# Optimization experiments

Measured on AMD Instinct MI355X. Metric: run time of the kernel, lower is better.

The kernel has to match this reference:

```python
import jax, jax.numpy as jnp
import numpy as np

NUM_PRIMITIVES = 1024
DIM = 1024
TAU = 0.5  # temperature used by LivingCodebook.discretize default


def setup_inputs() -> dict:
    key = jax.random.key(0)
    k1, k2 = jax.random.split(key)
    logits = jax.random.normal(k1, (8, 4096, NUM_PRIMITIVES), dtype=jnp.float32)
    # learned codebook (nn.Parameter torch.randn(K, D) * 0.02)
    primitives = jax.random.normal(k2, (NUM_PRIMITIVES, DIM), dtype=jnp.float32) * 0.02
    return {"logits": logits, "primitives": primitives}


def _gumbel_softmax_hard(logits, key, tau):
    # F.gumbel_softmax(logits, tau, hard=True): straight-through one-hot
    g = jax.random.gumbel(key, logits.shape, dtype=logits.dtype)
    y_soft = jax.nn.softmax((logits + g) / tau, axis=-1)  # [b,s,k]
    idx = jnp.argmax(y_soft, axis=-1)                     # [b,s]
    y_hard = jax.nn.one_hot(idx, logits.shape[-1], dtype=logits.dtype)
    # hard forward value, soft gradient
    y = y_hard + y_soft - jax.lax.stop_gradient(y_soft)
    return y, idx


def reference(logits, primitives):
    """LivingCodebook.discretize: hard gumbel-softmax selection + codebook gather
    (expressed as one-hot GEMM for straight-through grads), plus the
    activation_count update vectorized as a scatter-add."""
    noise_key = jax.random.key(42)
    weights, indices = _gumbel_softmax_hard(logits, noise_key, TAU)
    # embeddings = weights @ primitives : [b,s,k] x [k,d] -> [b,s,d]
    embeddings = jnp.einsum("bsk,kd->bsd", weights, primitives)
    # activation_count[idx] += 1 for every selected index (vectorized)
    counts = jnp.zeros((primitives.shape[0],), dtype=jnp.int32).at[indices.reshape(-1)].add(1)
    return embeddings, indices, counts
```

## Files before the change

### kernel.cpp

```cpp
#include <hip/hip_runtime.h>
#include <stdint.h>

#define NROWS   32768
#define KDIM    1024
#define IDX_OFF 33554432
#define CNT_OFF 33587200

__device__ __forceinline__ uint32_t rotl32(uint32_t x, int r) {
    return (x << r) | (x >> (32 - r));
}

__device__ __forceinline__ uint32_t threefry_bits(uint32_t ctr) {
    const uint32_t ks0 = 0u;
    const uint32_t ks1 = 42u;
    const uint32_t ks2 = 0x1BD11BDAu ^ 0u ^ 42u;

    uint32_t x0 = 0u + ks0;
    uint32_t x1 = ctr + ks1;

    x0 += x1; x1 = rotl32(x1, 13); x1 ^= x0;
    x0 += x1; x1 = rotl32(x1, 15); x1 ^= x0;
    x0 += x1; x1 = rotl32(x1, 26); x1 ^= x0;
    x0 += x1; x1 = rotl32(x1,  6); x1 ^= x0;
    x0 += ks1; x1 += ks2 + 1u;
    x0 += x1; x1 = rotl32(x1, 17); x1 ^= x0;
    x0 += x1; x1 = rotl32(x1, 29); x1 ^= x0;
    x0 += x1; x1 = rotl32(x1, 16); x1 ^= x0;
    x0 += x1; x1 = rotl32(x1, 24); x1 ^= x0;
    x0 += ks2; x1 += ks0 + 2u;
    x0 += x1; x1 = rotl32(x1, 13); x1 ^= x0;
    x0 += x1; x1 = rotl32(x1, 15); x1 ^= x0;
    x0 += x1; x1 = rotl32(x1, 26); x1 ^= x0;
    x0 += x1; x1 = rotl32(x1,  6); x1 ^= x0;
    x0 += ks0; x1 += ks1 + 3u;
    x0 += x1; x1 = rotl32(x1, 17); x1 ^= x0;
    x0 += x1; x1 = rotl32(x1, 29); x1 ^= x0;
    x0 += x1; x1 = rotl32(x1, 16); x1 ^= x0;
    x0 += x1; x1 = rotl32(x1, 24); x1 ^= x0;
    x0 += ks1; x1 += ks2 + 4u;
    x0 += x1; x1 = rotl32(x1, 13); x1 ^= x0;
    x0 += x1; x1 = rotl32(x1, 15); x1 ^= x0;
    x0 += x1; x1 = rotl32(x1, 26); x1 ^= x0;
    x0 += x1; x1 = rotl32(x1,  6); x1 ^= x0;
    x0 += ks2; x1 += ks0 + 5u;

    return x0 ^ x1;
}

__device__ __forceinline__ float score_from_bits(uint32_t bits, float logit) {
    float v1 = __uint_as_float((bits >> 9) | 0x3f800000u);
    float f  = v1 - 1.0f;
    float u  = fmaxf(f, 1.17549435e-38f);
    float w  = u - 1.0f;
    float q;
    q = fmaf(w, -0.20609929f,  0.24044917f);
    q = fmaf(w, q, -0.28853901f);
    q = fmaf(w, q,  0.36067376f);
    q = fmaf(w, q, -0.48089835f);
    q = fmaf(w, q,  0.72134752f);
    q = fmaf(w, q, -1.44269504f);
    float tp = w * q;
    float th = -__builtin_amdgcn_logf(u);
    float t  = (u >= 0.875f) ? tp : th;
    float lg = __builtin_amdgcn_logf(t);
    return fmaf(logit, 1.44269504f, -lg);
}

__global__ __launch_bounds__(256) void gumbel_argmax_gather(
    const float* __restrict__ logits,
    const float* __restrict__ prim,
    float* __restrict__ out)
{
    const int row = blockIdx.x;
    const int tid = threadIdx.x;
    const uint32_t base = (uint32_t)row * (uint32_t)KDIM;
    const uint32_t k0   = 4u * (uint32_t)tid;

    const float4 l4 = *reinterpret_cast<const float4*>(logits + base + k0);
    const float lv[4] = {l4.x, l4.y, l4.z, l4.w};

    float bv = -INFINITY;
    int   bk = 0;
    #pragma unroll
    for (int m = 0; m < 4; ++m) {
        const float z = score_from_bits(threefry_bits(base + k0 + (uint32_t)m), lv[m]);
        if (z > bv) { bv = z; bk = (int)k0 + m; }
    }

    #pragma unroll
    for (int off = 32; off > 0; off >>= 1) {
        const float ov = __shfl_down(bv, off);
        const int   ok = __shfl_down(bk, off);
        if (ov > bv || (ov == bv && ok < bk)) { bv = ov; bk = ok; }
    }

    __shared__ float s_v[4];
    __shared__ int   s_k[4];
    __shared__ int   s_idx;
    const int wave = tid >> 6;
    if ((tid & 63) == 0) { s_v[wave] = bv; s_k[wave] = bk; }
    __syncthreads();

    if (tid == 0) {
        float v = s_v[0]; int kk = s_k[0];
        #pragma unroll
        for (int w = 1; w < 4; ++w) {
            if (s_v[w] > v || (s_v[w] == v && s_k[w] < kk)) { v = s_v[w]; kk = s_k[w]; }
        }
        s_idx = kk;
        out[IDX_OFF + row] = (float)kk;
        atomicAdd(out + CNT_OFF + kk, 1.0f);
    }
    __syncthreads();

    const int idx = s_idx;
    const float4* __restrict__ src = (const float4*)(prim + (size_t)idx * KDIM);
    float4* __restrict__ dst = (float4*)(out + (size_t)row * KDIM);
    dst[tid] = src[tid];
}

extern "C" void kernel_launch(void* const* d_in, const int* in_sizes, int n_in,
                              void* d_out, int out_size, void* d_ws, size_t ws_size,
                              hipStream_t stream) {
    const float* logits = (const float*)d_in[0];
    const float* prim   = (const float*)d_in[1];
    float* out = (float*)d_out;
    (void)d_ws; (void)ws_size; (void)in_sizes; (void)n_in; (void)out_size;

    hipMemsetAsync(out + CNT_OFF, 0, KDIM * sizeof(float), stream);
    gumbel_argmax_gather<<<NROWS, 256, 0, stream>>>(logits, prim, out);
}
```

Before: 242.6 us.

## Assign one wavefront per row and drop block-level argmax synchronisation

Each 64-lane wavefront now processes a whole row: it scans all 1024 logits in four coalesced float4 passes and reduces with xor shuffles, so the shared-memory staging and both __syncthreads are gone. The grid shrinks to a quarter as many blocks, and every lane copies four float4 chunks of the selected codebook row. The uniform-variate math is also simplified, using an integer mantissa compare and computing w from v1 directly, which drops the fmax clamp. The cost is more serial work per thread and more registers, and the branch threshold and clamp semantics shift slightly for zero mantissas.

```diff
diff --git a/kernel.cpp b/kernel.cpp
--- a/kernel.cpp
+++ b/kernel.cpp
@@ -48,10 +48,10 @@
 }
 
 __device__ __forceinline__ float score_from_bits(uint32_t bits, float logit) {
-    float v1 = __uint_as_float((bits >> 9) | 0x3f800000u);
-    float f  = v1 - 1.0f;
-    float u  = fmaxf(f, 1.17549435e-38f);
-    float w  = u - 1.0f;
+    const uint32_t m  = bits >> 9;
+    const float    v1 = __uint_as_float(m | 0x3f800000u);
+    const float    u  = v1 - 1.0f;
+    const float    w  = v1 - 2.0f;
     float q;
     q = fmaf(w, -0.20609929f,  0.24044917f);
     q = fmaf(w, q, -0.28853901f);
@@ -59,10 +59,10 @@
     q = fmaf(w, q, -0.48089835f);
     q = fmaf(w, q,  0.72134752f);
     q = fmaf(w, q, -1.44269504f);
-    float tp = w * q;
-    float th = -__builtin_amdgcn_logf(u);
-    float t  = (u >= 0.875f) ? tp : th;
-    float lg = __builtin_amdgcn_logf(t);
+    const float tp = w * q;
+    const float th = -__builtin_amdgcn_logf(u);
+    const float t  = (m >= 0x00700000u) ? tp : th;
+    const float lg = __builtin_amdgcn_logf(t);
     return fmaf(logit, 1.44269504f, -lg);
 }
 
@@ -71,52 +71,52 @@
     const float* __restrict__ prim,
     float* __restrict__ out)
 {
-    const int row = blockIdx.x;
-    const int tid = threadIdx.x;
+    const int tid  = threadIdx.x;
+    const int lane = tid & 63;
+    const int wv   = tid >> 6;
+    const int row  = (blockIdx.x << 2) + wv;
     const uint32_t base = (uint32_t)row * (uint32_t)KDIM;
-    const uint32_t k0   = 4u * (uint32_t)tid;
 
-    const float4 l4 = *reinterpret_cast<const float4*>(logits + base + k0);
-    const float lv[4] = {l4.x, l4.y, l4.z, l4.w};
+    float bv[4] = {-INFINITY, -INFINITY, -INFINITY, -INFINITY};
+    int   bk[4] = {0, 0, 0, 0};
 
-    float bv = -INFINITY;
-    int   bk = 0;
     #pragma unroll
-    for (int m = 0; m < 4; ++m) {
-        const float z = score_from_bits(threefry_bits(base + k0 + (uint32_t)m), lv[m]);
-        if (z > bv) { bv = z; bk = (int)k0 + m; }
+    for (int j = 0; j < 4; ++j) {
+        const uint32_t k0 = (uint32_t)(j * 256 + lane * 4);
+        const float4 l4 = *reinterpret_cast<const float4*>(logits + base + k0);
+        const float lv[4] = {l4.x, l4.y, l4.z, l4.w};
+        #pragma unroll
+        for (int mm = 0; mm < 4; ++mm) {
+            const float z = score_from_bits(threefry_bits(base + k0 + (uint32_t)mm),
+                                            lv[mm]);
+            if (z > bv[mm]) { bv[mm] = z; bk[mm] = (int)(k0 + (uint32_t)mm); }
+        }
+    }
+
+    float v = bv[0]; int kk = bk[0];
+    #pragma unroll
+    for (int mm = 1; mm < 4; ++mm) {
+        if (bv[mm] > v || (bv[mm] == v && bk[mm] < kk)) { v = bv[mm]; kk = bk[mm]; }
     }
 
     #pragma unroll
-    for (int off = 32; off > 0; off >>= 1) {
-        const float ov = __shfl_down(bv, off);
-        const int   ok = __shfl_down(bk, off);
-        if (ov > bv || (ov == bv && ok < bk)) { bv = ov; bk = ok; }
+    for (int off = 1; off < 64; off <<= 1) {
+        const float ov = __shfl_xor(v, off);
+        const int   ok = __shfl_xor(kk, off);
+        if (ov > v || (ov == v && ok < kk)) { v = ov; kk = ok; }
     }
 
-    __shared__ float s_v[4];
-    __shared__ int   s_k[4];
-    __shared__ int   s_idx;
-    const int wave = tid >> 6;
-    if ((tid & 63) == 0) { s_v[wave] = bv; s_k[wave] = bk; }
-    __syncthreads();
-
-    if (tid == 0) {
-        float v = s_v[0]; int kk = s_k[0];
-        #pragma unroll
-        for (int w = 1; w < 4; ++w) {
-            if (s_v[w] > v || (s_v[w] == v && s_k[w] < kk)) { v = s_v[w]; kk = s_k[w]; }
-        }
-        s_idx = kk;
+    if (lane == 0) {
         out[IDX_OFF + row] = (float)kk;
         atomicAdd(out + CNT_OFF + kk, 1.0f);
     }
-    __syncthreads();
 
-    const int idx = s_idx;
-    const float4* __restrict__ src = (const float4*)(prim + (size_t)idx * KDIM);
+    const float4* __restrict__ src = (const float4*)(prim + (size_t)kk * KDIM);
     float4* __restrict__ dst = (float4*)(out + (size_t)row * KDIM);
-    dst[tid] = src[tid];
+    #pragma unroll
+    for (int it = 0; it < 4; ++it) {
+        dst[it * 64 + lane] = src[it * 64 + lane];
+    }
 }
 
 extern "C" void kernel_launch(void* const* d_in, const int* in_sizes, int n_in,
@@ -128,5 +128,5 @@
     (void)d_ws; (void)ws_size; (void)in_sizes; (void)n_in; (void)out_size;
 
     hipMemsetAsync(out + CNT_OFF, 0, KDIM * sizeof(float), stream);
-    gumbel_argmax_gather<<<NROWS, 256, 0, stream>>>(logits, prim, out);
+    gumbel_argmax_gather<<<NROWS / 4, 256, 0, stream>>>(logits, prim, out);
 }
```

Measured after the change: 235.6 us. 2.9% less time.
